# Optimization experiments

Measured on AMD Instinct MI355X. Metric: run time of the kernel, lower is better.

Reference implementation:

```python
import jax, jax.numpy as jnp
import numpy as np

PAD_ID = 12975
HEADS = 16


def _sinusoid_table(n_position, d_hid):
    # pos / 10000^(2*(j//2)/d_hid), sin on even dims, cos on odd dims
    pos = jnp.arange(n_position, dtype=jnp.float32)[:, None]          # [P,1]
    j = jnp.arange(d_hid)
    angle = pos / jnp.power(10000.0, (2.0 * (j // 2) / d_hid).astype(jnp.float32))  # [P,D]
    table = jnp.where((j % 2) == 0, jnp.sin(angle), jnp.cos(angle))
    return table  # [P, D]


def setup_inputs() -> dict:
    key = jax.random.key(0)
    k1, k2 = jax.random.split(key)
    x = jax.random.randint(k1, (256, 200), 0, 32000, dtype=jnp.int64)
    weight = jax.random.normal(k2, (32000, 1024), dtype=jnp.float32) * 0.02
    return {"x": x, "weight": weight}


def reference(x, weight):
    B, S = x.shape
    D = weight.shape[1]

    # --- mask build (faithful to the python-loop semantics) ---
    m = x == PAD_ID                                   # [B,S]
    has_pad = jnp.any(m, axis=1)                      # [B]
    first = jnp.argmax(m, axis=1)                     # first True index (0 if none)
    # torch loop: if no True found, i ends at S-1 and idx[S-1:] is still set True
    first = jnp.where(has_pad, first, S - 1)          # [B]
    row_ge = jnp.arange(S)[None, :] >= first[:, None]  # [B,S] rows >= first are all-True
    remask = m[:, None, :] | row_ge[:, :, None]       # [B,S,S]
    mask = jnp.broadcast_to(remask[:, None, :, :], (B, HEADS, S, S))  # [B,H,S,S]

    # --- embedding + sinusoidal positional encoding (dropout in eval = identity) ---
    emb = weight[x]                                   # [B,S,D]
    pos_table = _sinusoid_table(S, D)                 # [S,D]
    out = emb + pos_table[None, :, :]                 # [B,S,D]
    return (out, mask)
```

## Files before the change

kernel.cpp:

```cpp
#include <hip/hip_runtime.h>
#include <math.h>

#define PAD_ID 12975
#define BB 256
#define SS 200
#define DD 1024
#define HH 16

#define MASK_CHUNKS (BB * HH * SS * (SS / 4))
#define OUT_ROWS    (BB * SS)

#define NBLK 2048
#define MBLK 1280

typedef float f32x4 __attribute__((ext_vector_type(4)));
typedef int   i32x4 __attribute__((ext_vector_type(4)));

__global__ void work_kernel(const int* __restrict__ x, const float* __restrict__ weight,
                            float* __restrict__ out, float* __restrict__ mask) {
    if (blockIdx.x < MBLK) {
        __shared__ int sfirst[BB];
        {
            const int t = threadIdx.x;
            int f = SS - 1;
            const i32x4* xr = (const i32x4*)(x + t * SS);
            #pragma unroll 10
            for (int j4 = 49; j4 >= 0; --j4) {
                const i32x4 v = xr[j4];
                const int base = j4 * 4;
                if (v.w == PAD_ID) f = base + 3 < f ? base + 3 : f;
                if (v.z == PAD_ID) f = base + 2 < f ? base + 2 : f;
                if (v.y == PAD_ID) f = base + 1 < f ? base + 1 : f;
                if (v.x == PAD_ID) f = base + 0 < f ? base + 0 : f;
            }
            sfirst[t] = f;
        }
        __syncthreads();
        const int stride = MBLK * 256;
        for (int c = blockIdx.x * 256 + threadIdx.x; c < MASK_CHUNKS; c += stride) {
            const int row = c / 50;
            const int j4  = c - row * 50;
            const int b   = row / (HH * SS);
            const int i   = row % SS;
            f32x4 v;
            if (i >= sfirst[b]) {
                v = (f32x4){1.f, 1.f, 1.f, 1.f};
            } else {
                const i32x4 xv = ((const i32x4*)x)[b * 50 + j4];
                v.x = (xv.x == PAD_ID) ? 1.f : 0.f;
                v.y = (xv.y == PAD_ID) ? 1.f : 0.f;
                v.z = (xv.z == PAD_ID) ? 1.f : 0.f;
                v.w = (xv.w == PAD_ID) ? 1.f : 0.f;
            }
            __builtin_nontemporal_store(v, (f32x4*)mask + c);
        }
    } else {
        const int t = threadIdx.x;
        const float C = (float)(13.287712379549449 / 512.0);
        const float rd0 = exp2f(-(float)(2 * t) * C);
        const float rd1 = exp2f(-(float)(2 * t + 1) * C);
        const int ob = blockIdx.x - MBLK;
        const int OB = NBLK - MBLK;
        for (int row = ob; row < OUT_ROWS; row += OB) {
            const int s   = row % SS;
            const int idx = x[row];
            const float fs = (float)s;
            const float a0 = fs * rd0;
            const float a1 = fs * rd1;
            const f32x4 pe = (f32x4){sinf(a0), cosf(a0), sinf(a1), cosf(a1)};
            const f32x4 w = ((const f32x4*)(weight + (size_t)idx * DD))[t];
            __builtin_nontemporal_store(w + pe, (f32x4*)(out + (size_t)row * DD) + t);
        }
    }
}

extern "C" void kernel_launch(void* const* d_in, const int* in_sizes, int n_in,
                              void* d_out, int out_size, void* d_ws, size_t ws_size,
                              hipStream_t stream) {
    const int*   x      = (const int*)d_in[0];
    const float* weight = (const float*)d_in[1];
    float* out  = (float*)d_out;
    float* mask = out + (size_t)BB * SS * DD;

    work_kernel<<<NBLK, 256, 0, stream>>>(x, weight, out, mask);
}
```

Measured before the change: 172.4 us.

## Assign mask blocks per batch with shared pattern, use hardware sin/cos

Mask blocks are now assigned one batch row each, five blocks per batch. Each block computes its pad pattern and first-pad index once into shared memory with an atomicMin, instead of every block scanning all 256 rows and reloading x per chunk. The embedding path replaces sinf/cosf with range-reduced hardware sin/cos intrinsics, which may lose some accuracy for larger angles. The block split also changes, with 768 blocks for the embedding path and 1280 for the mask.

```diff
diff --git a/kernel.cpp b/kernel.cpp
--- a/kernel.cpp
+++ b/kernel.cpp
@@ -8,66 +8,75 @@
 #define HH 16
 
 #define MASK_CHUNKS (BB * HH * SS * (SS / 4))
-#define OUT_ROWS    (BB * SS)
+#define CHUNKS_PER_B (HH * SS * (SS / 4))
+#define BLKS_PER_B 5
+#define CHUNKS_PER_BLK (CHUNKS_PER_B / BLKS_PER_B)
 
-#define NBLK 2048
-#define MBLK 1280
+#define OUT_ROWS (BB * SS)
+
+#define MBLK (BB * BLKS_PER_B)
+#define OB   768
+#define NBLK (MBLK + OB)
 
 typedef float f32x4 __attribute__((ext_vector_type(4)));
 typedef int   i32x4 __attribute__((ext_vector_type(4)));
 
-__global__ void work_kernel(const int* __restrict__ x, const float* __restrict__ weight,
-                            float* __restrict__ out, float* __restrict__ mask) {
+__global__ void __launch_bounds__(256) work_kernel(const int* __restrict__ x,
+                                                   const float* __restrict__ weight,
+                                                   float* __restrict__ out,
+                                                   float* __restrict__ mask) {
     if (blockIdx.x < MBLK) {
-        __shared__ int sfirst[BB];
-        {
-            const int t = threadIdx.x;
-            int f = SS - 1;
-            const i32x4* xr = (const i32x4*)(x + t * SS);
-            #pragma unroll 10
-            for (int j4 = 49; j4 >= 0; --j4) {
-                const i32x4 v = xr[j4];
-                const int base = j4 * 4;
-                if (v.w == PAD_ID) f = base + 3 < f ? base + 3 : f;
-                if (v.z == PAD_ID) f = base + 2 < f ? base + 2 : f;
-                if (v.y == PAD_ID) f = base + 1 < f ? base + 1 : f;
-                if (v.x == PAD_ID) f = base + 0 < f ? base + 0 : f;
-            }
-            sfirst[t] = f;
+        const int b = blockIdx.x / BLKS_PER_B;
+        const int q = blockIdx.x - b * BLKS_PER_B;
+        __shared__ f32x4 pat[SS / 4];
+        __shared__ int   sfirst;
+        if (threadIdx.x == 0) sfirst = SS - 1;
+        __syncthreads();
+        if (threadIdx.x < SS / 4) {
+            const i32x4 xv = ((const i32x4*)(x + b * SS))[threadIdx.x];
+            f32x4 p;
+            p.x = (xv.x == PAD_ID) ? 1.f : 0.f;
+            p.y = (xv.y == PAD_ID) ? 1.f : 0.f;
+            p.z = (xv.z == PAD_ID) ? 1.f : 0.f;
+            p.w = (xv.w == PAD_ID) ? 1.f : 0.f;
+            pat[threadIdx.x] = p;
+            int f = 255;
+            if (xv.w == PAD_ID) f = threadIdx.x * 4 + 3;
+            if (xv.z == PAD_ID) f = threadIdx.x * 4 + 2;
+            if (xv.y == PAD_ID) f = threadIdx.x * 4 + 1;
+            if (xv.x == PAD_ID) f = threadIdx.x * 4 + 0;
+            atomicMin(&sfirst, f);
         }
         __syncthreads();
-        const int stride = MBLK * 256;
-        for (int c = blockIdx.x * 256 + threadIdx.x; c < MASK_CHUNKS; c += stride) {
-            const int row = c / 50;
-            const int j4  = c - row * 50;
-            const int b   = row / (HH * SS);
-            const int i   = row % SS;
-            f32x4 v;
-            if (i >= sfirst[b]) {
-                v = (f32x4){1.f, 1.f, 1.f, 1.f};
-            } else {
-                const i32x4 xv = ((const i32x4*)x)[b * 50 + j4];
-                v.x = (xv.x == PAD_ID) ? 1.f : 0.f;
-                v.y = (xv.y == PAD_ID) ? 1.f : 0.f;
-                v.z = (xv.z == PAD_ID) ? 1.f : 0.f;
-                v.w = (xv.w == PAD_ID) ? 1.f : 0.f;
-            }
-            __builtin_nontemporal_store(v, (f32x4*)mask + c);
+        const int first = sfirst;
+        const f32x4 ones = (f32x4){1.f, 1.f, 1.f, 1.f};
+        f32x4* const mptr = (f32x4*)mask + (size_t)b * CHUNKS_PER_B;
+        const int base = q * CHUNKS_PER_BLK;
+        for (int c = threadIdx.x; c < CHUNKS_PER_BLK; c += 256) {
+            const int d  = base + c;
+            const int r  = d / 50;
+            const int j4 = d - r * 50;
+            const int i  = r % SS;
+            const f32x4 v = (i >= first) ? ones : pat[j4];
+            __builtin_nontemporal_store(v, mptr + d);
         }
     } else {
         const int t = threadIdx.x;
         const float C = (float)(13.287712379549449 / 512.0);
         const float rd0 = exp2f(-(float)(2 * t) * C);
         const float rd1 = exp2f(-(float)(2 * t + 1) * C);
-        const int ob = blockIdx.x - MBLK;
-        const int OB = NBLK - MBLK;
-        for (int row = ob; row < OUT_ROWS; row += OB) {
+        const float INV2PI = 0.15915493667125702f;
+        for (int row = blockIdx.x - MBLK; row < OUT_ROWS; row += OB) {
             const int s   = row % SS;
             const int idx = x[row];
             const float fs = (float)s;
-            const float a0 = fs * rd0;
-            const float a1 = fs * rd1;
-            const f32x4 pe = (f32x4){sinf(a0), cosf(a0), sinf(a1), cosf(a1)};
+            float r0 = fs * rd0 * INV2PI;  r0 -= floorf(r0);
+            float r1 = fs * rd1 * INV2PI;  r1 -= floorf(r1);
+            f32x4 pe;
+            pe.x = __builtin_amdgcn_sinf(r0);
+            pe.y = __builtin_amdgcn_cosf(r0);
+            pe.z = __builtin_amdgcn_sinf(r1);
+            pe.w = __builtin_amdgcn_cosf(r1);
             const f32x4 w = ((const f32x4*)(weight + (size_t)idx * DD))[t];
             __builtin_nontemporal_store(w + pe, (f32x4*)(out + (size_t)row * DD) + t);
         }
```

After: 190.1 us. 10.3% more time.
